# Optimization experiments

Measured on AMD Instinct MI355X. Metric: run time of the kernel, lower is better.

Reference implementation:

```python
import jax, jax.numpy as jnp
import numpy as np

B, H, W, C = 8, 128, 128, 384
WS, SHIFT, NH = 8, 4, 12
N = WS * WS            # tokens per window = 64
HD = C // NH           # head dim = 32
SCALE = HD ** -0.5


def _rel_pos_index():
    ch, cw = np.meshgrid(np.arange(WS), np.arange(WS), indexing='ij')
    cf = np.stack([ch.ravel(), cw.ravel()])            # (2, N)
    rel = cf[:, :, None] - cf[:, None, :]              # (2, N, N)
    rel = rel.transpose(1, 2, 0)                       # (N, N, 2)
    rel[:, :, 0] += WS - 1
    rel[:, :, 1] += WS - 1
    rel[:, :, 0] *= 2 * WS - 1
    return jnp.asarray(rel.sum(-1))                    # (N, N) int

REL_IDX = _rel_pos_index()


def _shift_mask():
    # standard Swin SW-MSA mask, built once with numpy
    img = np.zeros((1, H, W, 1), np.float32)
    cnt = 0
    for hs in (slice(0, -WS), slice(-WS, -SHIFT), slice(-SHIFT, None)):
        for ws_ in (slice(0, -WS), slice(-WS, -SHIFT), slice(-SHIFT, None)):
            img[:, hs, ws_, :] = cnt
            cnt += 1
    m = img.reshape(1, H // WS, WS, W // WS, WS, 1).transpose(0, 1, 3, 2, 4, 5)
    m = m.reshape(-1, N)                               # (nW, N)
    am = m[:, None, :] - m[:, :, None]                 # (nW, N, N)
    return np.where(am != 0, np.float32(-100.0), np.float32(0.0))


def _ln(x, g, b, eps=1e-5):
    mu = x.mean(-1, keepdims=True)
    var = ((x - mu) ** 2).mean(-1, keepdims=True)
    return (x - mu) * jax.lax.rsqrt(var + eps) * g + b


def setup_inputs() -> dict:
    key = jax.random.key(0)
    ks = jax.random.split(key, 10)
    s = 0.02
    return {
        'x': jax.random.normal(ks[0], (B, H * W, C), jnp.float32),
        'qkv_w': jax.random.normal(ks[1], (3 * C, C), jnp.float32) * s,
        'qkv_b': jnp.zeros((3 * C,), jnp.float32),
        'proj_w': jax.random.normal(ks[2], (C, C), jnp.float32) * s,
        'proj_b': jnp.zeros((C,), jnp.float32),
        'rel_bias_table': jax.random.normal(ks[3], ((2 * WS - 1) ** 2, NH), jnp.float32) * s,
        'g1': jnp.ones((C,), jnp.float32), 'b1': jnp.zeros((C,), jnp.float32),
        'g2': jnp.ones((C,), jnp.float32), 'b2': jnp.zeros((C,), jnp.float32),
        'fc1_w': jax.random.normal(ks[4], (4 * C, C), jnp.float32) * s,
        'fc1_b': jnp.zeros((4 * C,), jnp.float32),
        'fc2_w': jax.random.normal(ks[5], (C, 4 * C), jnp.float32) * s,
        'fc2_b': jnp.zeros((C,), jnp.float32),
        'attn_mask': jnp.asarray(_shift_mask()),       # (nW, N, N)
    }


def reference(x, qkv_w, qkv_b, proj_w, proj_b, rel_bias_table, g1, b1, g2, b2,
              fc1_w, fc1_b, fc2_w, fc2_b, attn_mask):
    shortcut = x
    h = _ln(x, g1, b1).reshape(B, H, W, C)
    # cyclic shift (SW-MSA)
    h = jnp.roll(h, (-SHIFT, -SHIFT), axis=(1, 2))
    # window partition -> (B*nW, N, C)
    nWh, nWw = H // WS, W // WS
    hw = h.reshape(B, nWh, WS, nWw, WS, C).transpose(0, 1, 3, 2, 4, 5)
    hw = hw.reshape(B * nWh * nWw, N, C)
    # qkv projection
    qkv = jnp.einsum('bnc,dc->bnd', hw, qkv_w) + qkv_b   # (Bw, N, 3C)
    qkv = qkv.reshape(-1, N, 3, NH, HD).transpose(2, 0, 3, 1, 4)
    q, k, v = qkv[0], qkv[1], qkv[2]                    # (Bw, NH, N, HD)
    attn = jnp.einsum('bhnd,bhmd->bhnm', q * SCALE, k)  # (Bw, NH, N, N)
    bias = rel_bias_table[REL_IDX.reshape(-1)].reshape(N, N, NH)
    attn = attn + bias.transpose(2, 0, 1)[None]
    # shift mask: attn viewed as (B, nW, NH, N, N) + mask (nW, 1, N, N)
    nW = nWh * nWw
    attn = attn.reshape(B, nW, NH, N, N) + attn_mask[None, :, None]
    attn = jax.nn.softmax(attn.reshape(-1, NH, N, N), axis=-1)
    out = jnp.einsum('bhnm,bhmd->bnhd', attn, v).reshape(-1, N, C)
    out = jnp.einsum('bnc,dc->bnd', out, proj_w) + proj_b
    # window reverse + un-shift
    out = out.reshape(B, nWh, nWw, WS, WS, C).transpose(0, 1, 3, 2, 4, 5)
    out = out.reshape(B, H, W, C)
    out = jnp.roll(out, (SHIFT, SHIFT), axis=(1, 2)).reshape(B, H * W, C)
    x = shortcut + out
    # MLP block
    h2 = _ln(x, g2, b2)
    h2 = jax.nn.gelu(jnp.einsum('blc,dc->bld', h2, fc1_w) + fc1_b, approximate=False)
    h2 = jnp.einsum('bld,cd->blc', h2, fc2_w) + fc2_b
    return x + h2
```

## Files before the change

kernel.cpp:

```cpp
#include <hip/hip_runtime.h>
#include <hip/hip_bf16.h>
#include <math.h>

typedef __attribute__((ext_vector_type(4))) float f32x4;
typedef __attribute__((ext_vector_type(8))) short bf16x8;

__device__ __forceinline__ unsigned short f2bf(float f) {
  unsigned int x = __builtin_bit_cast(unsigned int, f);
  x += 0x7fffu + ((x >> 16) & 1u);
  return (unsigned short)(x >> 16);
}
__device__ __forceinline__ float bf2f(unsigned short u) {
  unsigned int x = ((unsigned int)u) << 16;
  return __builtin_bit_cast(float, x);
}

__device__ __forceinline__ void gload_lds16(const void* g, void* l) {
  __builtin_amdgcn_global_load_lds(
      (const __attribute__((address_space(1))) unsigned int*)g,
      (__attribute__((address_space(3))) unsigned int*)l, 16, 0, 0);
}

__global__ void cvt_all(const float* __restrict__ s0, int n0, const float* __restrict__ s1, int n1,
                        const float* __restrict__ s2, int n2, const float* __restrict__ s3, int n3,
                        unsigned short* __restrict__ d) {
  int i = blockIdx.x * 256 + threadIdx.x;
  if (i >= n0 + n1 + n2 + n3) return;
  const float* s;
  int off;
  if (i < n0) { s = s0; off = 0; }
  else if (i < n0 + n1) { s = s1; off = n0; }
  else if (i < n0 + n1 + n2) { s = s2; off = n0 + n1; }
  else { s = s3; off = n0 + n1 + n2; }
  d[i] = f2bf(s[i - off]);
}

template <int REMAP>
__global__ __launch_bounds__(256)
void ln_kernel(const float* __restrict__ x, const float* __restrict__ g,
               const float* __restrict__ b, unsigned short* __restrict__ dst_o) {
  int r = blockIdx.x * 4 + (threadIdx.x >> 6);
  int lane = threadIdx.x & 63;
  size_t src;
  if (REMAP) {
    int w = r >> 6, t = r & 63;
    int bb = w >> 8, wi = (w >> 4) & 15, wj = w & 15;
    int i = t >> 3, j = t & 7;
    int p = (wi * 8 + i + 4) & 127, q = (wj * 8 + j + 4) & 127;
    src = ((size_t)bb * 16384 + p * 128 + q) * 384;
  } else {
    src = (size_t)r * 384;
  }
  float v[6];
  float s = 0.f, s2 = 0.f;
#pragma unroll
  for (int m = 0; m < 6; ++m) {
    v[m] = x[src + lane + 64 * m];
    s += v[m];
    s2 += v[m] * v[m];
  }
#pragma unroll
  for (int o2 = 1; o2 < 64; o2 <<= 1) {
    s += __shfl_xor(s, o2);
    s2 += __shfl_xor(s2, o2);
  }
  float mu = s * (1.f / 384.f);
  float var = s2 * (1.f / 384.f) - mu * mu;
  float ri = rsqrtf(var + 1e-5f);
  size_t dst = (size_t)r * 384;
#pragma unroll
  for (int m = 0; m < 6; ++m) {
    int c = lane + 64 * m;
    dst_o[dst + c] = f2bf((v[m] - mu) * ri * g[c] + b[c]);
  }
}

__global__ __launch_bounds__(256)
void ln_bf16(const unsigned short* __restrict__ x, const float* __restrict__ g,
             const float* __restrict__ b, unsigned short* __restrict__ dst_o) {
  int r = blockIdx.x * 4 + (threadIdx.x >> 6);
  int lane = threadIdx.x & 63;
  size_t src = (size_t)r * 384;
  float v[6];
  float s = 0.f, s2 = 0.f;
#pragma unroll
  for (int m = 0; m < 3; ++m) {
    unsigned int u = *(const unsigned int*)&x[src + lane * 2 + 128 * m];
    v[2 * m] = bf2f((unsigned short)(u & 0xffffu));
    v[2 * m + 1] = bf2f((unsigned short)(u >> 16));
    s += v[2 * m] + v[2 * m + 1];
    s2 += v[2 * m] * v[2 * m] + v[2 * m + 1] * v[2 * m + 1];
  }
#pragma unroll
  for (int o2 = 1; o2 < 64; o2 <<= 1) {
    s += __shfl_xor(s, o2);
    s2 += __shfl_xor(s2, o2);
  }
  float mu = s * (1.f / 384.f);
  float var = s2 * (1.f / 384.f) - mu * mu;
  float ri = rsqrtf(var + 1e-5f);
#pragma unroll
  for (int m = 0; m < 3; ++m) {
    int c = lane * 2 + 128 * m;
    unsigned int lo = f2bf((v[2 * m] - mu) * ri * g[c] + b[c]);
    unsigned int hi = f2bf((v[2 * m + 1] - mu) * ri * g[c + 1] + b[c + 1]);
    *(unsigned int*)&dst_o[src + c] = lo | (hi << 16);
  }
}

template <int EPI>
__global__ __launch_bounds__(512, 1)
void gemm9(const unsigned short* __restrict__ A, const unsigned short* __restrict__ Bw,
           const float* __restrict__ bias, int M, int N, int K, int NT,
           unsigned short* __restrict__ Obf, const void* __restrict__ resid,
           float* __restrict__ Of) {
  extern __shared__ unsigned short lds[];
  const int tid = threadIdx.x;
  const int lane = tid & 63;
  const int wid = tid >> 6;
  const int wm = wid >> 1, wn = wid & 1;
  const int li = lane & 15, lg = lane >> 4;

  const int nwg = gridDim.x;
  const int orig = blockIdx.x;
  const int q = nwg >> 3, r = nwg & 7;
  const int xcd = orig & 7, loc = orig >> 3;
  const int wg = (xcd < r ? xcd * (q + 1) : r * (q + 1) + (xcd - r) * q) + loc;
  const int m0 = (wg / NT) * 256;
  const int n0 = (wg % NT) * 192;

  const int srow = wid * 8 + (lane >> 3);
  const int scol = ((lane & 7) ^ (lane >> 3)) * 8;
  const unsigned short* gA = A + (size_t)(m0 + srow) * K + scol;
  const unsigned short* gB = Bw + (size_t)(n0 + srow) * K + scol;

  const int nk = K >> 6;
  const int fswz = (li & 7) << 3;
  f32x4 acc[4][6] = {};

  auto stage = [&](int k, unsigned short* dst) {
    unsigned short* dB = dst + 16384;
#pragma unroll
    for (int c = 0; c < 4; ++c)
      gload_lds16(gA + (size_t)(c * 64) * K + k * 64, &dst[c * 4096 + wid * 512]);
#pragma unroll
    for (int c = 0; c < 3; ++c)
      gload_lds16(gB + (size_t)(c * 64) * K + k * 64, &dB[c * 4096 + wid * 512]);
  };

  unsigned short* const buf0 = lds;
  unsigned short* const buf1 = lds + 28672;

  auto tile = [&](int t, unsigned short* cur, unsigned short* nxt) {
    if (t + 1 < nk) stage(t + 1, nxt);
    const unsigned short* pA = cur;
    const unsigned short* pB = cur + 16384;
#pragma unroll
    for (int kk = 0; kk < 2; ++kk) {
      bf16x8 a[4], b[6];
#pragma unroll
      for (int f = 0; f < 4; ++f)
        a[f] = *(const bf16x8*)&pA[(wm * 64 + f * 16 + li) * 64 + ((kk * 32 + lg * 8) ^ fswz)];
#pragma unroll
      for (int f = 0; f < 6; ++f)
        b[f] = *(const bf16x8*)&pB[(wn * 96 + f * 16 + li) * 64 + ((kk * 32 + lg * 8) ^ fswz)];
      __builtin_amdgcn_s_barrier();
      __builtin_amdgcn_s_setprio(1);
#pragma unroll
      for (int mf = 0; mf < 4; ++mf)
#pragma unroll
        for (int nf = 0; nf < 6; ++nf)
          acc[mf][nf] = __builtin_amdgcn_mfma_f32_16x16x32_bf16(a[mf], b[nf], acc[mf][nf], 0, 0, 0);
      __builtin_amdgcn_s_setprio(0);
      if (kk == 0) __builtin_amdgcn_s_barrier();
    }
    asm volatile("s_waitcnt vmcnt(0)" ::: "memory");
    __builtin_amdgcn_s_barrier();
  };

  stage(0, buf0);
  asm volatile("s_waitcnt vmcnt(0)" ::: "memory");
  __builtin_amdgcn_s_barrier();

  for (int t = 0; t < nk; t += 2) {
    tile(t, buf0, buf1);
    tile(t + 1, buf1, buf0);
  }

#pragma unroll
  for (int mf = 0; mf < 4; ++mf) {
#pragma unroll
    for (int r2 = 0; r2 < 4; ++r2) {
      int mrow = m0 + wm * 64 + mf * 16 + lg * 4 + r2;
      size_t orow = (size_t)mrow;
      if (EPI == 2) {
        int w = mrow >> 6, t = mrow & 63;
        int bb2 = w >> 8, wi = (w >> 4) & 15, wj = w & 15;
        int i = t >> 3, j = t & 7;
        int p = (wi * 8 + i + 4) & 127, qq = (wj * 8 + j + 4) & 127;
        orow = (size_t)bb2 * 16384 + p * 128 + qq;
      }
#pragma unroll
      for (int nf = 0; nf < 6; ++nf) {
        int col = n0 + wn * 96 + nf * 16 + li;
        float v = acc[mf][nf][r2] + bias[col];
        if (EPI == 0) {
          Obf[(size_t)mrow * N + col] = f2bf(v);
        } else if (EPI == 1) {
          float y = 1.5957691f * (v + 0.044715f * v * v * v);
          float gl = v * __builtin_amdgcn_rcpf(1.f + __expf(-y));
          Obf[(size_t)mrow * N + col] = f2bf(gl);
        } else if (EPI == 2) {
          const float* rx = (const float*)resid;
          Obf[orow * 384 + col] = f2bf(v + rx[orow * 384 + col]);
        } else {
          const unsigned short* rx = (const unsigned short*)resid;
          Of[(size_t)mrow * N + col] = v + bf2f(rx[(size_t)mrow * N + col]);
        }
      }
    }
  }
}

__global__ __launch_bounds__(256, 2)
void attn_kernel(const unsigned short* __restrict__ qkv, const float* __restrict__ btab,
                 const float* __restrict__ mask, unsigned short* __restrict__ out) {
  __shared__ unsigned short v_lds[4][64 * 40];
  __shared__ unsigned short p_lds[4][64 * 72];
  const int w = blockIdx.x;
  const int hi = blockIdx.y;
  const int tid = threadIdx.x;
  const int wid = tid >> 6, lane = tid & 63;
  const int li = lane & 15, lg = lane >> 4;
  const float* mrow = mask + (size_t)(w & 255) * 4096;
  const size_t base = (size_t)w * 64;
  const float SC = 0.17677669529663688f;

  int h = wid * 3 + hi;
  bf16x8 aq[4], bk[4];
#pragma unroll
  for (int f = 0; f < 4; ++f) {
    size_t off = (base + f * 16 + li) * 1152 + h * 32 + lg * 8;
    aq[f] = *(const bf16x8*)&qkv[off];
    bk[f] = *(const bf16x8*)&qkv[off + 384];
  }
  f32x4 s[4][4] = {};
#pragma unroll
  for (int mf = 0; mf < 4; ++mf)
#pragma unroll
    for (int nf = 0; nf < 4; ++nf)
      s[mf][nf] = __builtin_amdgcn_mfma_f32_16x16x32_bf16(aq[mf], bk[nf], s[mf][nf], 0, 0, 0);

  {
    const unsigned short* vp = &qkv[(base + lane) * 1152 + 768 + h * 32];
    unsigned short* dp = &v_lds[wid][lane * 40];
#pragma unroll
    for (int c = 0; c < 4; ++c) *(bf16x8*)&dp[c * 8] = *(const bf16x8*)&vp[c * 8];
  }

#pragma unroll
  for (int mf = 0; mf < 4; ++mf) {
#pragma unroll
    for (int r = 0; r < 4; ++r) {
      int m = mf * 16 + lg * 4 + r;
      float mx = -1e30f;
#pragma unroll
      for (int nf = 0; nf < 4; ++nf) {
        int n = nf * 16 + li;
        int ridx = ((m >> 3) - (n >> 3) + 7) * 15 + (m & 7) - (n & 7) + 7;
        float val = s[mf][nf][r] * SC + btab[ridx * 12 + h] + mrow[m * 64 + n];
        s[mf][nf][r] = val;
        mx = fmaxf(mx, val);
      }
#pragma unroll
      for (int o2 = 1; o2 < 16; o2 <<= 1) mx = fmaxf(mx, __shfl_xor(mx, o2));
      float sum = 0.f;
#pragma unroll
      for (int nf = 0; nf < 4; ++nf) {
        float e = __expf(s[mf][nf][r] - mx);
        s[mf][nf][r] = e;
        sum += e;
      }
#pragma unroll
      for (int o2 = 1; o2 < 16; o2 <<= 1) sum += __shfl_xor(sum, o2);
      float inv = __builtin_amdgcn_rcpf(sum);
#pragma unroll
      for (int nf = 0; nf < 4; ++nf) s[mf][nf][r] *= inv;
    }
  }

#pragma unroll
  for (int mf = 0; mf < 4; ++mf)
#pragma unroll
    for (int nf = 0; nf < 4; ++nf)
#pragma unroll
      for (int r = 0; r < 4; ++r) {
        int m = mf * 16 + lg * 4 + r, n = nf * 16 + li;
        p_lds[wid][m * 72 + n] = f2bf(s[mf][nf][r]);
      }

  f32x4 o[4][2] = {};
#pragma unroll
  for (int kf = 0; kf < 2; ++kf) {
    bf16x8 bv[2];
#pragma unroll
    for (int df = 0; df < 2; ++df) {
      bf16x8 t;
#pragma unroll
      for (int e = 0; e < 8; ++e)
        t[e] = (short)v_lds[wid][(kf * 32 + lg * 8 + e) * 40 + df * 16 + li];
      bv[df] = t;
    }
#pragma unroll
    for (int mf = 0; mf < 4; ++mf) {
      bf16x8 pa = *(const bf16x8*)&p_lds[wid][(mf * 16 + li) * 72 + kf * 32 + lg * 8];
#pragma unroll
      for (int df = 0; df < 2; ++df)
        o[mf][df] = __builtin_amdgcn_mfma_f32_16x16x32_bf16(pa, bv[df], o[mf][df], 0, 0, 0);
    }
  }

#pragma unroll
  for (int mf = 0; mf < 4; ++mf)
#pragma unroll
    for (int df = 0; df < 2; ++df)
#pragma unroll
      for (int r = 0; r < 4; ++r) {
        size_t row = base + mf * 16 + lg * 4 + r;
        out[row * 384 + h * 32 + df * 16 + li] = f2bf(o[mf][df][r]);
      }
}

extern "C" void kernel_launch(void* const* d_in, const int* in_sizes, int n_in,
                              void* d_out, int out_size, void* d_ws, size_t ws_size,
                              hipStream_t stream) {
  const float* x      = (const float*)d_in[0];
  const float* qkv_w  = (const float*)d_in[1];
  const float* qkv_b  = (const float*)d_in[2];
  const float* proj_w = (const float*)d_in[3];
  const float* proj_b = (const float*)d_in[4];
  const float* rel    = (const float*)d_in[5];
  const float* g1     = (const float*)d_in[6];
  const float* b1     = (const float*)d_in[7];
  const float* g2     = (const float*)d_in[8];
  const float* b2     = (const float*)d_in[9];
  const float* fc1_w  = (const float*)d_in[10];
  const float* fc1_b  = (const float*)d_in[11];
  const float* fc2_w  = (const float*)d_in[12];
  const float* fc2_b  = (const float*)d_in[13];
  const float* mask   = (const float*)d_in[14];
  float* out = (float*)d_out;
  char* ws = (char*)d_ws;

  const int M = 131072;
  const int LDS_BYTES = 2 * 57344;
  (void)hipFuncSetAttribute((const void*)gemm9<0>, hipFuncAttributeMaxDynamicSharedMemorySize, LDS_BYTES);
  (void)hipFuncSetAttribute((const void*)gemm9<1>, hipFuncAttributeMaxDynamicSharedMemorySize, LDS_BYTES);
  (void)hipFuncSetAttribute((const void*)gemm9<2>, hipFuncAttributeMaxDynamicSharedMemorySize, LDS_BYTES);
  (void)hipFuncSetAttribute((const void*)gemm9<3>, hipFuncAttributeMaxDynamicSharedMemorySize, LDS_BYTES);

  unsigned short* hw     = (unsigned short*)ws;
  unsigned short* qkv    = (unsigned short*)(ws + 100663296);
  unsigned short* hmid   = (unsigned short*)ws;
  unsigned short* attn_o = (unsigned short*)(ws + 402653184);
  unsigned short* ln2o   = attn_o;
  unsigned short* x1b    = (unsigned short*)(ws + 503316480);
  unsigned short* wq     = (unsigned short*)(ws + 603979776);
  unsigned short* wp     = wq + 442368;
  unsigned short* w1     = wp + 147456;
  unsigned short* w2     = w1 + 589824;

  cvt_all<<<(442368 + 147456 + 589824 + 589824 + 255) / 256, 256, 0, stream>>>(
      qkv_w, 442368, proj_w, 147456, fc1_w, 589824, fc2_w, 589824, wq);

  ln_kernel<1><<<M / 4, 256, 0, stream>>>(x, g1, b1, hw);

  gemm9<0><<<512 * 6, 512, LDS_BYTES, stream>>>(hw, wq, qkv_b, M, 1152, 384, 6, qkv, nullptr, nullptr);

  attn_kernel<<<dim3(2048, 3), 256, 0, stream>>>(qkv, rel, mask, attn_o);

  gemm9<2><<<512 * 2, 512, LDS_BYTES, stream>>>(attn_o, wp, proj_b, M, 384, 384, 2, x1b, x, nullptr);

  ln_bf16<<<M / 4, 256, 0, stream>>>(x1b, g2, b2, ln2o);

  gemm9<1><<<512 * 8, 512, LDS_BYTES, stream>>>(ln2o, w1, fc1_b, M, 1536, 384, 8, hmid, nullptr, nullptr);

  gemm9<3><<<512 * 2, 512, LDS_BYTES, stream>>>(hmid, w2, fc2_b, M, 384, 1536, 2, nullptr, x1b, out);
}
```

Measured before the change: 1.147 ms.

## Replace LDS-staged GEMM with direct global-to-register loads and bf16 residual

Rewrites the GEMM kernel to drop LDS staging. Each wave now loads its A/B MFMA fragments directly from global memory into registers, double-buffered in registers, with smaller 128-row workgroups of 4 waves and 2 blocks per CU. The first LayerNorm also writes a bf16 copy of the input so the projection epilogue reads a bf16 residual instead of fp32. The aim is to remove LDS traffic and barriers and to halve residual bytes. The cost is redundant global/L2 reads of operands across waves and reduced residual precision.

```diff
diff --git a/kernel.cpp b/kernel.cpp
--- a/kernel.cpp
+++ b/kernel.cpp
@@ -13,12 +13,6 @@
 __device__ __forceinline__ float bf2f(unsigned short u) {
   unsigned int x = ((unsigned int)u) << 16;
   return __builtin_bit_cast(float, x);
-}
-
-__device__ __forceinline__ void gload_lds16(const void* g, void* l) {
-  __builtin_amdgcn_global_load_lds(
-      (const __attribute__((address_space(1))) unsigned int*)g,
-      (__attribute__((address_space(3))) unsigned int*)l, 16, 0, 0);
 }
 
 __global__ void cvt_all(const float* __restrict__ s0, int n0, const float* __restrict__ s1, int n1,
@@ -38,7 +32,8 @@
 template <int REMAP>
 __global__ __launch_bounds__(256)
 void ln_kernel(const float* __restrict__ x, const float* __restrict__ g,
-               const float* __restrict__ b, unsigned short* __restrict__ dst_o) {
+               const float* __restrict__ b, unsigned short* __restrict__ dst_o,
+               unsigned short* __restrict__ xb) {
   int r = blockIdx.x * 4 + (threadIdx.x >> 6);
   int lane = threadIdx.x & 63;
   size_t src;
@@ -59,6 +54,10 @@
     s += v[m];
     s2 += v[m] * v[m];
   }
+  if (REMAP) {
+#pragma unroll
+    for (int m = 0; m < 6; ++m) xb[src + lane + 64 * m] = f2bf(v[m]);
+  }
 #pragma unroll
   for (int o2 = 1; o2 < 64; o2 <<= 1) {
     s += __shfl_xor(s, o2);
@@ -109,12 +108,11 @@
 }
 
 template <int EPI>
-__global__ __launch_bounds__(512, 1)
-void gemm9(const unsigned short* __restrict__ A, const unsigned short* __restrict__ Bw,
+__global__ __launch_bounds__(256, 2)
+void gemmR(const unsigned short* __restrict__ A, const unsigned short* __restrict__ Bw,
            const float* __restrict__ bias, int M, int N, int K, int NT,
-           unsigned short* __restrict__ Obf, const void* __restrict__ resid,
+           unsigned short* __restrict__ Obf, const unsigned short* __restrict__ resid,
            float* __restrict__ Of) {
-  extern __shared__ unsigned short lds[];
   const int tid = threadIdx.x;
   const int lane = tid & 63;
   const int wid = tid >> 6;
@@ -126,65 +124,49 @@
   const int q = nwg >> 3, r = nwg & 7;
   const int xcd = orig & 7, loc = orig >> 3;
   const int wg = (xcd < r ? xcd * (q + 1) : r * (q + 1) + (xcd - r) * q) + loc;
-  const int m0 = (wg / NT) * 256;
+  const int m0 = (wg / NT) * 128;
   const int n0 = (wg % NT) * 192;
 
-  const int srow = wid * 8 + (lane >> 3);
-  const int scol = ((lane & 7) ^ (lane >> 3)) * 8;
-  const unsigned short* gA = A + (size_t)(m0 + srow) * K + scol;
-  const unsigned short* gB = Bw + (size_t)(n0 + srow) * K + scol;
-
-  const int nk = K >> 6;
-  const int fswz = (li & 7) << 3;
+  const unsigned short* pa[4];
+  const unsigned short* pb[6];
+#pragma unroll
+  for (int f = 0; f < 4; ++f) pa[f] = A + (size_t)(m0 + wm * 64 + f * 16 + li) * K + lg * 8;
+#pragma unroll
+  for (int f = 0; f < 6; ++f) pb[f] = Bw + (size_t)(n0 + wn * 96 + f * 16 + li) * K + lg * 8;
+
   f32x4 acc[4][6] = {};
-
-  auto stage = [&](int k, unsigned short* dst) {
-    unsigned short* dB = dst + 16384;
-#pragma unroll
-    for (int c = 0; c < 4; ++c)
-      gload_lds16(gA + (size_t)(c * 64) * K + k * 64, &dst[c * 4096 + wid * 512]);
-#pragma unroll
-    for (int c = 0; c < 3; ++c)
-      gload_lds16(gB + (size_t)(c * 64) * K + k * 64, &dB[c * 4096 + wid * 512]);
-  };
-
-  unsigned short* const buf0 = lds;
-  unsigned short* const buf1 = lds + 28672;
-
-  auto tile = [&](int t, unsigned short* cur, unsigned short* nxt) {
-    if (t + 1 < nk) stage(t + 1, nxt);
-    const unsigned short* pA = cur;
-    const unsigned short* pB = cur + 16384;
-#pragma unroll
-    for (int kk = 0; kk < 2; ++kk) {
-      bf16x8 a[4], b[6];
-#pragma unroll
-      for (int f = 0; f < 4; ++f)
-        a[f] = *(const bf16x8*)&pA[(wm * 64 + f * 16 + li) * 64 + ((kk * 32 + lg * 8) ^ fswz)];
-#pragma unroll
-      for (int f = 0; f < 6; ++f)
-        b[f] = *(const bf16x8*)&pB[(wn * 96 + f * 16 + li) * 64 + ((kk * 32 + lg * 8) ^ fswz)];
-      __builtin_amdgcn_s_barrier();
-      __builtin_amdgcn_s_setprio(1);
-#pragma unroll
-      for (int mf = 0; mf < 4; ++mf)
-#pragma unroll
-        for (int nf = 0; nf < 6; ++nf)
-          acc[mf][nf] = __builtin_amdgcn_mfma_f32_16x16x32_bf16(a[mf], b[nf], acc[mf][nf], 0, 0, 0);
-      __builtin_amdgcn_s_setprio(0);
-      if (kk == 0) __builtin_amdgcn_s_barrier();
-    }
-    asm volatile("s_waitcnt vmcnt(0)" ::: "memory");
-    __builtin_amdgcn_s_barrier();
-  };
-
-  stage(0, buf0);
-  asm volatile("s_waitcnt vmcnt(0)" ::: "memory");
-  __builtin_amdgcn_s_barrier();
-
-  for (int t = 0; t < nk; t += 2) {
-    tile(t, buf0, buf1);
-    tile(t + 1, buf1, buf0);
+  bf16x8 a0[4], b0[6], a1[4], b1[6];
+
+  const int ns = K >> 5;
+
+#pragma unroll
+  for (int f = 0; f < 4; ++f) a0[f] = *(const bf16x8*)(pa[f]);
+#pragma unroll
+  for (int f = 0; f < 6; ++f) b0[f] = *(const bf16x8*)(pb[f]);
+
+  for (int s = 0; s < ns; s += 2) {
+    if (s + 1 < ns) {
+#pragma unroll
+      for (int f = 0; f < 4; ++f) a1[f] = *(const bf16x8*)(pa[f] + (s + 1) * 32);
+#pragma unroll
+      for (int f = 0; f < 6; ++f) b1[f] = *(const bf16x8*)(pb[f] + (s + 1) * 32);
+    }
+#pragma unroll
+    for (int mf = 0; mf < 4; ++mf)
+#pragma unroll
+      for (int nf = 0; nf < 6; ++nf)
+        acc[mf][nf] = __builtin_amdgcn_mfma_f32_16x16x32_bf16(a0[mf], b0[nf], acc[mf][nf], 0, 0, 0);
+    if (s + 2 < ns) {
+#pragma unroll
+      for (int f = 0; f < 4; ++f) a0[f] = *(const bf16x8*)(pa[f] + (s + 2) * 32);
+#pragma unroll
+      for (int f = 0; f < 6; ++f) b0[f] = *(const bf16x8*)(pb[f] + (s + 2) * 32);
+    }
+#pragma unroll
+    for (int mf = 0; mf < 4; ++mf)
+#pragma unroll
+      for (int nf = 0; nf < 6; ++nf)
+        acc[mf][nf] = __builtin_amdgcn_mfma_f32_16x16x32_bf16(a1[mf], b1[nf], acc[mf][nf], 0, 0, 0);
   }
 
 #pragma unroll
@@ -211,11 +193,9 @@
           float gl = v * __builtin_amdgcn_rcpf(1.f + __expf(-y));
           Obf[(size_t)mrow * N + col] = f2bf(gl);
         } else if (EPI == 2) {
-          const float* rx = (const float*)resid;
-          Obf[orow * 384 + col] = f2bf(v + rx[orow * 384 + col]);
+          Obf[orow * 384 + col] = f2bf(v + bf2f(resid[orow * 384 + col]));
         } else {
-          const unsigned short* rx = (const unsigned short*)resid;
-          Of[(size_t)mrow * N + col] = v + bf2f(rx[(size_t)mrow * N + col]);
+          Of[(size_t)mrow * N + col] = v + bf2f(resid[(size_t)mrow * N + col]);
         }
       }
     }
@@ -353,12 +333,6 @@
   char* ws = (char*)d_ws;
 
   const int M = 131072;
-  const int LDS_BYTES = 2 * 57344;
-  (void)hipFuncSetAttribute((const void*)gemm9<0>, hipFuncAttributeMaxDynamicSharedMemorySize, LDS_BYTES);
-  (void)hipFuncSetAttribute((const void*)gemm9<1>, hipFuncAttributeMaxDynamicSharedMemorySize, LDS_BYTES);
-  (void)hipFuncSetAttribute((const void*)gemm9<2>, hipFuncAttributeMaxDynamicSharedMemorySize, LDS_BYTES);
-  (void)hipFuncSetAttribute((const void*)gemm9<3>, hipFuncAttributeMaxDynamicSharedMemorySize, LDS_BYTES);
-
   unsigned short* hw     = (unsigned short*)ws;
   unsigned short* qkv    = (unsigned short*)(ws + 100663296);
   unsigned short* hmid   = (unsigned short*)ws;
@@ -369,21 +343,22 @@
   unsigned short* wp     = wq + 442368;
   unsigned short* w1     = wp + 147456;
   unsigned short* w2     = w1 + 589824;
+  unsigned short* xb     = (unsigned short*)(ws + 607518720);
 
   cvt_all<<<(442368 + 147456 + 589824 + 589824 + 255) / 256, 256, 0, stream>>>(
       qkv_w, 442368, proj_w, 147456, fc1_w, 589824, fc2_w, 589824, wq);
 
-  ln_kernel<1><<<M / 4, 256, 0, stream>>>(x, g1, b1, hw);
-
-  gemm9<0><<<512 * 6, 512, LDS_BYTES, stream>>>(hw, wq, qkv_b, M, 1152, 384, 6, qkv, nullptr, nullptr);
+  ln_kernel<1><<<M / 4, 256, 0, stream>>>(x, g1, b1, hw, xb);
+
+  gemmR<0><<<1024 * 6, 256, 0, stream>>>(hw, wq, qkv_b, M, 1152, 384, 6, qkv, nullptr, nullptr);
 
   attn_kernel<<<dim3(2048, 3), 256, 0, stream>>>(qkv, rel, mask, attn_o);
 
-  gemm9<2><<<512 * 2, 512, LDS_BYTES, stream>>>(attn_o, wp, proj_b, M, 384, 384, 2, x1b, x, nullptr);
+  gemmR<2><<<1024 * 2, 256, 0, stream>>>(attn_o, wp, proj_b, M, 384, 384, 2, x1b, xb, nullptr);
 
   ln_bf16<<<M / 4, 256, 0, stream>>>(x1b, g2, b2, ln2o);
 
-  gemm9<1><<<512 * 8, 512, LDS_BYTES, stream>>>(ln2o, w1, fc1_b, M, 1536, 384, 8, hmid, nullptr, nullptr);
-
-  gemm9<3><<<512 * 2, 512, LDS_BYTES, stream>>>(hmid, w2, fc2_b, M, 384, 1536, 2, nullptr, x1b, out);
-}
+  gemmR<1><<<1024 * 8, 256, 0, stream>>>(ln2o, w1, fc1_b, M, 1536, 384, 8, hmid, nullptr, nullptr);
+
+  gemmR<3><<<1024 * 2, 256, 0, stream>>>(hmid, w2, fc2_b, M, 384, 1536, 2, nullptr, x1b, out);
+}
```

New measurement: 1.870 ms. +63.1%, slower.
